# Kernel optimization log

Measured on AMD Instinct MI355X. Metric: run time of the kernel, lower is better.

## Reference

```python
import jax, jax.numpy as jnp
import numpy as np


def setup_inputs() -> dict:
    key = jax.random.key(0)
    ks = jax.random.split(key, 9)
    B, H = 8192, 1024
    scale = 1.0 / np.sqrt(4 * H)
    return {
        "h": jax.random.normal(ks[0], (B, H), jnp.float32),
        "x": jax.random.normal(ks[1], (B, 2 * H), jnp.float32),
        "glo": jax.random.normal(ks[2], (B, H), jnp.float32),
        "Wi_w": jax.random.normal(ks[3], (H, 4 * H), jnp.float32) * scale,
        "Wi_b": jnp.zeros((H,), jnp.float32),
        "Wf_w": jax.random.normal(ks[4], (H, 4 * H), jnp.float32) * scale,
        "Wf_b": jnp.zeros((H,), jnp.float32),
        "Wc_w": jax.random.normal(ks[5], (H, 4 * H), jnp.float32) * scale,
        "Wc_b": jnp.zeros((H,), jnp.float32),
    }


def reference(h, x, glo, Wi_w, Wi_b, Wf_w, Wf_b, Wc_w, Wc_b):
    # Dropout is identity in eval mode (deterministic reference).
    cat_all = jnp.concatenate([h, x, glo], axis=-1)  # [B, 4H]
    # Fused gate GEMM: stack the three weight matrices, one matmul.
    W = jnp.concatenate([Wi_w, Wf_w, Wc_w], axis=0)      # [3H, 4H]
    b = jnp.concatenate([Wi_b, Wf_b, Wc_b], axis=0)      # [3H]
    gates = cat_all @ W.T + b                             # [B, 3H]
    H = h.shape[-1]
    i = jax.nn.sigmoid(gates[:, :H])
    f = jax.nn.sigmoid(gates[:, H:2 * H])
    c = jnp.tanh(gates[:, 2 * H:])
    # 2-way softmax over (i, f): alpha0 = exp(i)/(exp(i)+exp(f)) = sigmoid(i-f)
    alpha0 = jax.nn.sigmoid(i - f)
    output = alpha0 * c + (1.0 - alpha0) * h
    return output
```

## Files before the change

kernel.cpp:

```cpp
#include <hip/hip_runtime.h>

typedef unsigned short USHORT;
typedef short bf16x8 __attribute__((ext_vector_type(8)));
typedef float f32x4 __attribute__((ext_vector_type(4)));

__device__ __forceinline__ USHORT f2bf(float f) {
    unsigned u = __float_as_uint(f);
    u += 0x7fffu + ((u >> 16) & 1u);
    return (USHORT)(u >> 16);
}
__device__ __forceinline__ float bf2f(USHORT s) {
    return __uint_as_float(((unsigned)s) << 16);
}
__device__ __forceinline__ float sigm(float v) { return 1.f / (1.f + __expf(-v)); }
__device__ __forceinline__ float mytanh(float v) { return 1.f - 2.f / (__expf(2.f * v) + 1.f); }

using gcu32p = const unsigned int __attribute__((address_space(1))) *;
using lu32p  = unsigned int __attribute__((address_space(3))) *;

__device__ __forceinline__ void load_lds16(const void* g, void* l) {
    __builtin_amdgcn_global_load_lds((gcu32p)g, (lu32p)l, 16, 0, 0);
}

__global__ __launch_bounds__(256) void conv_all(const float* __restrict__ h,
                                                const float* __restrict__ x,
                                                const float* __restrict__ glo,
                                                const float* __restrict__ Wi,
                                                const float* __restrict__ Wf,
                                                const float* __restrict__ Wc,
                                                USHORT* __restrict__ A,
                                                USHORT* __restrict__ W) {
    int bid = blockIdx.x;
    if (bid < 16384) {
        int idx = (bid * 256 + threadIdx.x) * 8;
        int m = idx >> 12, k = idx & 4095;
        const float* s;
        if (k < 1024)      s = h   + (size_t)m * 1024 + k;
        else if (k < 3072) s = x   + (size_t)m * 2048 + (k - 1024);
        else               s = glo + (size_t)m * 1024 + (k - 3072);
        float4 f0 = ((const float4*)s)[0];
        float4 f1 = ((const float4*)s)[1];
        union { USHORT us[8]; uint4 v; } u;
        u.us[0] = f2bf(f0.x); u.us[1] = f2bf(f0.y); u.us[2] = f2bf(f0.z); u.us[3] = f2bf(f0.w);
        u.us[4] = f2bf(f1.x); u.us[5] = f2bf(f1.y); u.us[6] = f2bf(f1.z); u.us[7] = f2bf(f1.w);
        *(uint4*)(A + idx) = u.v;
    } else {
        int idx = ((bid - 16384) * 256 + threadIdx.x) * 8;
        int n = idx >> 12, k = idx & 4095;
        const float* base = (n < 1024) ? Wi : (n < 2048 ? Wf : Wc);
        const float* s = base + (size_t)(n & 1023) * 4096 + k;
        float4 f0 = ((const float4*)s)[0];
        float4 f1 = ((const float4*)s)[1];
        union { USHORT us[8]; uint4 v; } u;
        u.us[0] = f2bf(f0.x); u.us[1] = f2bf(f0.y); u.us[2] = f2bf(f0.z); u.us[3] = f2bf(f0.w);
        u.us[4] = f2bf(f1.x); u.us[5] = f2bf(f1.y); u.us[6] = f2bf(f1.z); u.us[7] = f2bf(f1.w);
        *(uint4*)(W + idx) = u.v;
    }
}


#define A_ELEMS 16384
#define B_ELEMS 12288

template<int AISS, int BISS, int WMODE>
__device__ __forceinline__ void do_tile(int par, USHORT* As, USHORT* Bs,
                                        const USHORT* (&aG)[4], const USHORT* (&bG)[3],
                                        int wvOff, int aOff, int bOff, int koff0,
                                        f32x4 (&acc)[8][3]) {
    const USHORT* aRdp = As + par * A_ELEMS + aOff;
    const USHORT* bRdp = Bs + par * B_ELEMS + bOff;
    bf16x8 bv[3][2];
    #pragma unroll
    for (int q = 0; q < 4; ++q) {
        bf16x8 av[2][2];
        #pragma unroll
        for (int m2 = 0; m2 < 2; ++m2)
            #pragma unroll
            for (int kh = 0; kh < 2; ++kh)
                av[m2][kh] = *(const bf16x8*)(aRdp + (q * 32 + m2 * 16) * 64 + (koff0 ^ (kh * 32)));
        if (q == 0) {
            #pragma unroll
            for (int nt = 0; nt < 3; ++nt)
                #pragma unroll
                for (int kh = 0; kh < 2; ++kh)
                    bv[nt][kh] = *(const bf16x8*)(bRdp + nt * 16 * 64 + (koff0 ^ (kh * 32)));
        }
        if (AISS && q < 2) {
            int j = q * 2;
            load_lds16(aG[j],     As + (par ^ 1) * A_ELEMS + j * 4096 + wvOff);
            load_lds16(aG[j + 1], As + (par ^ 1) * A_ELEMS + (j + 1) * 4096 + wvOff);
            aG[j] += 64; aG[j + 1] += 64;
        }
        if (BISS && q == 2) {
            load_lds16(bG[0], Bs + par * B_ELEMS + 0    + wvOff);
            load_lds16(bG[1], Bs + par * B_ELEMS + 4096 + wvOff);
            bG[0] += 64; bG[1] += 64;
        }
        if (BISS && q == 3) {
            load_lds16(bG[2], Bs + par * B_ELEMS + 8192 + wvOff);
            bG[2] += 64;
        }
        __builtin_amdgcn_sched_barrier(0);
        __builtin_amdgcn_s_barrier();
        __builtin_amdgcn_s_setprio(1);
        #pragma unroll
        for (int m2 = 0; m2 < 2; ++m2)
            #pragma unroll
            for (int nt = 0; nt < 3; ++nt)
                #pragma unroll
                for (int kh = 0; kh < 2; ++kh)
                    acc[q * 2 + m2][nt] = __builtin_amdgcn_mfma_f32_16x16x32_bf16(
                        av[m2][kh], bv[nt][kh], acc[q * 2 + m2][nt], 0, 0, 0);
        __builtin_amdgcn_s_setprio(0);
        if (q == 3) {
            if (WMODE == 0) asm volatile("s_waitcnt vmcnt(3)" ::: "memory");
            else if (WMODE == 1) asm volatile("s_waitcnt vmcnt(0)" ::: "memory");
        }
        __builtin_amdgcn_s_barrier();
    }
}

__global__ __launch_bounds__(512, 2) void gemm8p(const USHORT* __restrict__ A,
                                                 const USHORT* __restrict__ B,
                                                 const float* __restrict__ bi,
                                                 const float* __restrict__ bfp,
                                                 const float* __restrict__ bc,
                                                 USHORT* __restrict__ gates) {
    __shared__ __align__(16) USHORT As[2 * 256 * 64];
    __shared__ __align__(16) USHORT Bs[2 * 192 * 64];

    const int tid  = threadIdx.x;
    const int lane = tid & 63, wv = tid >> 6;
    const int s  = (blockIdx.x & 7) * 64 + (blockIdx.x >> 3);
    const int m0 = (s & 31) * 256;
    const int n0 = (s >> 5) * 192;

    const int wM = wv >> 2, wN = wv & 3;
    const int lm = lane & 15;
    const int gw = lane >> 4;
    const int koff0 = ((gw ^ (lm >> 1)) & 7) * 8;
    const int wvOff = wv * 512;
    const int aOff = (wM * 128 + lm) * 64;
    const int bOff = (wN * 48 + lm) * 64;

    const int gswz = ((lane & 7) ^ (4 * (wv & 1) + (lane >> 4))) & 7;
    const USHORT* aG[4];
    const USHORT* bG[3];
    #pragma unroll
    for (int j = 0; j < 4; ++j)
        aG[j] = A + (size_t)(m0 + j * 64 + wv * 8 + (lane >> 3)) * 4096 + gswz * 8;
    #pragma unroll
    for (int t = 0; t < 3; ++t)
        bG[t] = B + (size_t)(n0 + t * 64 + wv * 8 + (lane >> 3)) * 4096 + gswz * 8;

    f32x4 acc[8][3];
    #pragma unroll
    for (int a = 0; a < 8; ++a)
        #pragma unroll
        for (int b = 0; b < 3; ++b) {
            f32x4 z = {0.f, 0.f, 0.f, 0.f};
            acc[a][b] = z;
        }

    #pragma unroll
    for (int j = 0; j < 4; ++j) { load_lds16(aG[j], As + j * 4096 + wvOff); aG[j] += 64; }
    #pragma unroll
    for (int t = 0; t < 3; ++t) { load_lds16(bG[t], Bs + t * 4096 + wvOff); bG[t] += 64; }
    #pragma unroll
    for (int t = 0; t < 3; ++t) { load_lds16(bG[t], Bs + B_ELEMS + t * 4096 + wvOff); bG[t] += 64; }
    asm volatile("s_waitcnt vmcnt(3)" ::: "memory");
    __builtin_amdgcn_s_barrier();

    #pragma unroll 2
    for (int kt = 0; kt < 62; ++kt)
        do_tile<1, 1, 0>(kt & 1, As, Bs, aG, bG, wvOff, aOff, bOff, koff0, acc);
    do_tile<1, 0, 1>(0, As, Bs, aG, bG, wvOff, aOff, bOff, koff0, acc);
    do_tile<0, 0, 2>(1, As, Bs, aG, bG, wvOff, aOff, bOff, koff0, acc);

    #pragma unroll
    for (int nt = 0; nt < 3; ++nt) {
        int gc = n0 + wN * 48 + nt * 16 + lm;
        float bb = (gc < 1024) ? bi[gc] : (gc < 2048 ? bfp[gc - 1024] : bc[gc - 2048]);
        #pragma unroll
        for (int mt = 0; mt < 8; ++mt) {
            #pragma unroll
            for (int r = 0; r < 4; ++r) {
                int lrow = wM * 128 + mt * 16 + (lane >> 4) * 4 + r;
                gates[(size_t)(m0 + lrow) * 3072 + gc] = f2bf(acc[mt][nt][r] + bb);
            }
        }
    }
}

__global__ __launch_bounds__(256) void epi(const USHORT* __restrict__ gates,
                                           const float* __restrict__ h,
                                           float* __restrict__ out) {
    int e = (blockIdx.x * 256 + threadIdx.x) * 8;
    int m = e >> 10, n = e & 1023;
    const USHORT* gp = gates + (size_t)m * 3072 + n;
    union { USHORT us[8]; uint4 v; } gi, gf, gc;
    gi.v = *(const uint4*)(gp);
    gf.v = *(const uint4*)(gp + 1024);
    gc.v = *(const uint4*)(gp + 2048);
    const float* hp = h + (size_t)m * 1024 + n;
    float4 h0 = ((const float4*)hp)[0];
    float4 h1 = ((const float4*)hp)[1];
    float hv[8] = {h0.x, h0.y, h0.z, h0.w, h1.x, h1.y, h1.z, h1.w};
    float o[8];
    #pragma unroll
    for (int j = 0; j < 8; ++j) {
        float iv = sigm(bf2f(gi.us[j]));
        float fv = sigm(bf2f(gf.us[j]));
        float cv = mytanh(bf2f(gc.us[j]));
        float al = sigm(iv - fv);
        o[j] = al * cv + (1.f - al) * hv[j];
    }
    float4* op = (float4*)(out + (size_t)m * 1024 + n);
    op[0] = make_float4(o[0], o[1], o[2], o[3]);
    op[1] = make_float4(o[4], o[5], o[6], o[7]);
}

__global__ __launch_bounds__(256) void gemm3_noconv(const float* __restrict__ h,
                                                    const float* __restrict__ x,
                                                    const float* __restrict__ glo,
                                                    const float* __restrict__ Wi,
                                                    const float* __restrict__ Wf,
                                                    const float* __restrict__ Wc,
                                                    const float* __restrict__ bi,
                                                    const float* __restrict__ bfp,
                                                    const float* __restrict__ bc,
                                                    float* __restrict__ out) {
    __shared__ USHORT At[128 * 32];
    __shared__ USHORT Bt[128 * 32];
    __shared__ USHORT stash[128 * 136];

    const int tid  = threadIdx.x;
    const int lane = tid & 63, wv = tid >> 6;
    const int n0 = blockIdx.x * 128;
    const int m0 = blockIdx.y * 128;
    const int wM = wv >> 1, wN = wv & 1;
    const int lm = lane & 15, qk = (lane >> 4) * 8;
    const int rowS = tid >> 1;
    const int colS = (tid & 1) * 16;

    for (int p = 0; p < 3; ++p) {
        f32x4 acc[4][4];
        #pragma unroll
        for (int a = 0; a < 4; ++a)
            #pragma unroll
            for (int b = 0; b < 4; ++b) {
                f32x4 z = {0.f, 0.f, 0.f, 0.f};
                acc[a][b] = z;
            }
        const float* Wg = (p == 0) ? Wi : (p == 1 ? Wf : Wc);

        for (int kt = 0; kt < 128; ++kt) {
            __syncthreads();
            int k = kt * 32 + colS;
            const float* s;
            if (k < 1024)      s = h   + (size_t)(m0 + rowS) * 1024 + k;
            else if (k < 3072) s = x   + (size_t)(m0 + rowS) * 2048 + (k - 1024);
            else               s = glo + (size_t)(m0 + rowS) * 1024 + (k - 3072);
            float4 f0 = ((const float4*)s)[0], f1 = ((const float4*)s)[1];
            float4 f2 = ((const float4*)s)[2], f3 = ((const float4*)s)[3];
            union { USHORT us[8]; uint4 v; } u0, u1;
            u0.us[0]=f2bf(f0.x); u0.us[1]=f2bf(f0.y); u0.us[2]=f2bf(f0.z); u0.us[3]=f2bf(f0.w);
            u0.us[4]=f2bf(f1.x); u0.us[5]=f2bf(f1.y); u0.us[6]=f2bf(f1.z); u0.us[7]=f2bf(f1.w);
            u1.us[0]=f2bf(f2.x); u1.us[1]=f2bf(f2.y); u1.us[2]=f2bf(f2.z); u1.us[3]=f2bf(f2.w);
            u1.us[4]=f2bf(f3.x); u1.us[5]=f2bf(f3.y); u1.us[6]=f2bf(f3.z); u1.us[7]=f2bf(f3.w);
            *(uint4*)(At + rowS * 32 + colS)     = u0.v;
            *(uint4*)(At + rowS * 32 + colS + 8) = u1.v;
            const float* sw = Wg + (size_t)(n0 + rowS) * 4096 + k;
            float4 w0 = ((const float4*)sw)[0], w1 = ((const float4*)sw)[1];
            float4 w2 = ((const float4*)sw)[2], w3 = ((const float4*)sw)[3];
            union { USHORT us[8]; uint4 v; } v0, v1;
            v0.us[0]=f2bf(w0.x); v0.us[1]=f2bf(w0.y); v0.us[2]=f2bf(w0.z); v0.us[3]=f2bf(w0.w);
            v0.us[4]=f2bf(w1.x); v0.us[5]=f2bf(w1.y); v0.us[6]=f2bf(w1.z); v0.us[7]=f2bf(w1.w);
            v1.us[0]=f2bf(w2.x); v1.us[1]=f2bf(w2.y); v1.us[2]=f2bf(w2.z); v1.us[3]=f2bf(w2.w);
            v1.us[4]=f2bf(w3.x); v1.us[5]=f2bf(w3.y); v1.us[6]=f2bf(w3.z); v1.us[7]=f2bf(w3.w);
            *(uint4*)(Bt + rowS * 32 + colS)     = v0.v;
            *(uint4*)(Bt + rowS * 32 + colS + 8) = v1.v;
            __syncthreads();

            bf16x8 av[4], bv[4];
            #pragma unroll
            for (int mt = 0; mt < 4; ++mt)
                av[mt] = *(const bf16x8*)(At + (wM * 64 + mt * 16 + lm) * 32 + qk);
            #pragma unroll
            for (int nt = 0; nt < 4; ++nt)
                bv[nt] = *(const bf16x8*)(Bt + (wN * 64 + nt * 16 + lm) * 32 + qk);
            #pragma unroll
            for (int mt = 0; mt < 4; ++mt)
                #pragma unroll
                for (int nt = 0; nt < 4; ++nt)
                    acc[mt][nt] = __builtin_amdgcn_mfma_f32_16x16x32_bf16(
                        av[mt], bv[nt], acc[mt][nt], 0, 0, 0);
        }

        const float* bias = (p == 0) ? bi : (p == 1 ? bfp : bc);
        #pragma unroll
        for (int nt = 0; nt < 4; ++nt) {
            int lcol = wN * 64 + nt * 16 + lm;
            float bb = bias[n0 + lcol];
            #pragma unroll
            for (int mt = 0; mt < 4; ++mt) {
                #pragma unroll
                for (int r = 0; r < 4; ++r) {
                    int lrow = wM * 64 + mt * 16 + (lane >> 4) * 4 + r;
                    float g = acc[mt][nt][r] + bb;
                    int li = lrow * 136 + lcol;
                    if (p == 0) {
                        stash[li] = f2bf(sigm(g));
                    } else if (p == 1) {
                        float iv = bf2f(stash[li]);
                        stash[li] = f2bf(sigm(iv - sigm(g)));
                    } else {
                        float al = bf2f(stash[li]);
                        float cv = mytanh(g);
                        size_t gi = (size_t)(m0 + lrow) * 1024 + (n0 + lcol);
                        out[gi] = al * cv + (1.f - al) * h[gi];
                    }
                }
            }
        }
    }
}

extern "C" void kernel_launch(void* const* d_in, const int* in_sizes, int n_in,
                              void* d_out, int out_size, void* d_ws, size_t ws_size,
                              hipStream_t stream) {
    const float* h   = (const float*)d_in[0];
    const float* x   = (const float*)d_in[1];
    const float* glo = (const float*)d_in[2];
    const float* Wi  = (const float*)d_in[3];
    const float* bi  = (const float*)d_in[4];
    const float* Wf  = (const float*)d_in[5];
    const float* bfp = (const float*)d_in[6];
    const float* Wc  = (const float*)d_in[7];
    const float* bc  = (const float*)d_in[8];
    float* out = (float*)d_out;

    const size_t szA = (size_t)8192 * 4096 * 2;
    const size_t szW = (size_t)3072 * 4096 * 2;
    const size_t szG = (size_t)8192 * 3072 * 2;

    if (ws_size >= szA + szW + szG) {
        USHORT* Abf = (USHORT*)d_ws;
        USHORT* Wbf = (USHORT*)((char*)d_ws + szA);
        USHORT* Gbf = (USHORT*)((char*)d_ws + szA + szW);
        conv_all<<<16384 + 6144, 256, 0, stream>>>(h, x, glo, Wi, Wf, Wc, Abf, Wbf);
        gemm8p<<<512, 512, 0, stream>>>(Abf, Wbf, bi, bfp, bc, Gbf);
        epi<<<4096, 256, 0, stream>>>(Gbf, h, out);
    } else {
        gemm3_noconv<<<dim3(8, 64), 256, 0, stream>>>(
            h, x, glo, Wi, Wf, Wc, bi, bfp, bc, out);
    }
}
```

Before: 461.2 us.

## Triple-buffer A tiles in LDS to prefetch two K-steps ahead

```diff
diff --git a/kernel.cpp b/kernel.cpp
--- a/kernel.cpp
+++ b/kernel.cpp
@@ -62,13 +62,11 @@
 #define A_ELEMS 16384
 #define B_ELEMS 12288
 
-template<int AISS, int BISS, int WMODE>
-__device__ __forceinline__ void do_tile(int par, USHORT* As, USHORT* Bs,
+template<int ISS, int WMODE>
+__device__ __forceinline__ void do_tile(const USHORT* aRd, const USHORT* bRd,
+                                        USHORT* aWr, USHORT* bWr,
                                         const USHORT* (&aG)[4], const USHORT* (&bG)[3],
-                                        int wvOff, int aOff, int bOff, int koff0,
-                                        f32x4 (&acc)[8][3]) {
-    const USHORT* aRdp = As + par * A_ELEMS + aOff;
-    const USHORT* bRdp = Bs + par * B_ELEMS + bOff;
+                                        int koff0, f32x4 (&acc)[8][3]) {
     bf16x8 bv[3][2];
     #pragma unroll
     for (int q = 0; q < 4; ++q) {
@@ -77,28 +75,31 @@
         for (int m2 = 0; m2 < 2; ++m2)
             #pragma unroll
             for (int kh = 0; kh < 2; ++kh)
-                av[m2][kh] = *(const bf16x8*)(aRdp + (q * 32 + m2 * 16) * 64 + (koff0 ^ (kh * 32)));
+                av[m2][kh] = *(const bf16x8*)(aRd + (q * 32 + m2 * 16) * 64 + (koff0 ^ (kh * 32)));
         if (q == 0) {
             #pragma unroll
             for (int nt = 0; nt < 3; ++nt)
                 #pragma unroll
                 for (int kh = 0; kh < 2; ++kh)
-                    bv[nt][kh] = *(const bf16x8*)(bRdp + nt * 16 * 64 + (koff0 ^ (kh * 32)));
-        }
-        if (AISS && q < 2) {
-            int j = q * 2;
-            load_lds16(aG[j],     As + (par ^ 1) * A_ELEMS + j * 4096 + wvOff);
-            load_lds16(aG[j + 1], As + (par ^ 1) * A_ELEMS + (j + 1) * 4096 + wvOff);
-            aG[j] += 64; aG[j + 1] += 64;
-        }
-        if (BISS && q == 2) {
-            load_lds16(bG[0], Bs + par * B_ELEMS + 0    + wvOff);
-            load_lds16(bG[1], Bs + par * B_ELEMS + 4096 + wvOff);
-            bG[0] += 64; bG[1] += 64;
-        }
-        if (BISS && q == 3) {
-            load_lds16(bG[2], Bs + par * B_ELEMS + 8192 + wvOff);
-            bG[2] += 64;
+                    bv[nt][kh] = *(const bf16x8*)(bRd + nt * 16 * 64 + (koff0 ^ (kh * 32)));
+        }
+        if (ISS) {
+            if (q == 0) {
+                load_lds16(aG[0], aWr);
+                load_lds16(aG[1], aWr + 4096);
+                aG[0] += 64; aG[1] += 64;
+            } else if (q == 1) {
+                load_lds16(aG[2], aWr + 8192);
+                load_lds16(aG[3], aWr + 12288);
+                aG[2] += 64; aG[3] += 64;
+            } else if (q == 2) {
+                load_lds16(bG[0], bWr);
+                load_lds16(bG[1], bWr + 4096);
+                bG[0] += 64; bG[1] += 64;
+            } else {
+                load_lds16(bG[2], bWr + 8192);
+                bG[2] += 64;
+            }
         }
         __builtin_amdgcn_sched_barrier(0);
         __builtin_amdgcn_s_barrier();
@@ -113,7 +114,7 @@
                         av[m2][kh], bv[nt][kh], acc[q * 2 + m2][nt], 0, 0, 0);
         __builtin_amdgcn_s_setprio(0);
         if (q == 3) {
-            if (WMODE == 0) asm volatile("s_waitcnt vmcnt(3)" ::: "memory");
+            if (WMODE == 0) asm volatile("s_waitcnt vmcnt(7)" ::: "memory");
             else if (WMODE == 1) asm volatile("s_waitcnt vmcnt(0)" ::: "memory");
         }
         __builtin_amdgcn_s_barrier();
@@ -126,7 +127,7 @@
                                                  const float* __restrict__ bfp,
                                                  const float* __restrict__ bc,
                                                  USHORT* __restrict__ gates) {
-    __shared__ __align__(16) USHORT As[2 * 256 * 64];
+    __shared__ __align__(16) USHORT As[3 * 256 * 64];
     __shared__ __align__(16) USHORT Bs[2 * 192 * 64];
 
     const int tid  = threadIdx.x;
@@ -162,20 +163,31 @@
             acc[a][b] = z;
         }
 
-    #pragma unroll
-    for (int j = 0; j < 4; ++j) { load_lds16(aG[j], As + j * 4096 + wvOff); aG[j] += 64; }
-    #pragma unroll
-    for (int t = 0; t < 3; ++t) { load_lds16(bG[t], Bs + t * 4096 + wvOff); bG[t] += 64; }
-    #pragma unroll
-    for (int t = 0; t < 3; ++t) { load_lds16(bG[t], Bs + B_ELEMS + t * 4096 + wvOff); bG[t] += 64; }
-    asm volatile("s_waitcnt vmcnt(3)" ::: "memory");
+    USHORT* aB0 = As;
+    USHORT* aB1 = As + A_ELEMS;
+    USHORT* aB2 = As + 2 * A_ELEMS;
+    USHORT* bB0 = Bs;
+    USHORT* bB1 = Bs + B_ELEMS;
+
+    #pragma unroll
+    for (int j = 0; j < 4; ++j) { load_lds16(aG[j], aB0 + j * 4096 + wvOff); aG[j] += 64; }
+    #pragma unroll
+    for (int t = 0; t < 3; ++t) { load_lds16(bG[t], bB0 + t * 4096 + wvOff); bG[t] += 64; }
+    #pragma unroll
+    for (int j = 0; j < 4; ++j) { load_lds16(aG[j], aB1 + j * 4096 + wvOff); aG[j] += 64; }
+    #pragma unroll
+    for (int t = 0; t < 3; ++t) { load_lds16(bG[t], bB1 + t * 4096 + wvOff); bG[t] += 64; }
+    asm volatile("s_waitcnt vmcnt(7)" ::: "memory");
     __builtin_amdgcn_s_barrier();
 
-    #pragma unroll 2
-    for (int kt = 0; kt < 62; ++kt)
-        do_tile<1, 1, 0>(kt & 1, As, Bs, aG, bG, wvOff, aOff, bOff, koff0, acc);
-    do_tile<1, 0, 1>(0, As, Bs, aG, bG, wvOff, aOff, bOff, koff0, acc);
-    do_tile<0, 0, 2>(1, As, Bs, aG, bG, wvOff, aOff, bOff, koff0, acc);
+    for (int kt = 0; kt < 62; ++kt) {
+        do_tile<1, 0>(aB0 + aOff, bB0 + bOff, aB2 + wvOff, bB0 + wvOff,
+                      aG, bG, koff0, acc);
+        USHORT* tp = aB0; aB0 = aB1; aB1 = aB2; aB2 = tp;
+        tp = bB0; bB0 = bB1; bB1 = tp;
+    }
+    do_tile<0, 1>(aB0 + aOff, bB0 + bOff, As, Bs, aG, bG, koff0, acc);
+    do_tile<0, 2>(aB1 + aOff, bB1 + bOff, As, Bs, aG, bG, koff0, acc);
 
     #pragma unroll
     for (int nt = 0; nt < 3; ++nt) {
```

Result: faster. 448.2 us (-2.8%).
